# Kernel optimization log

Measured on AMD Instinct MI355X. Metric: run time of the kernel, lower is better.

Reference implementation:

```python
import jax, jax.numpy as jnp
import numpy as np

_DIMS = [15, 30, 60, 90, 120, 90, 60, 30, 15, 10, 5, 1]


def setup_inputs() -> dict:
    key = jax.random.key(0)
    keys = jax.random.split(key, 1 + 2 * 11)
    inp = {"x": jax.random.normal(keys[0], (524288, 15), dtype=jnp.float32)}
    for i in range(11):
        fan_in, fan_out = _DIMS[i], _DIMS[i + 1]
        bound = 1.0 / np.sqrt(fan_in)
        inp[f"W{i+1}"] = jax.random.uniform(keys[1 + 2 * i], (fan_out, fan_in), minval=-bound, maxval=bound, dtype=jnp.float32)
        inp[f"b{i+1}"] = jax.random.uniform(keys[2 + 2 * i], (fan_out,), minval=-bound, maxval=bound, dtype=jnp.float32)
    return inp


def reference(x, W1, b1, W2, b2, W3, b3, W4, b4, W5, b5, W6, b6, W7, b7, W8, b8, W9, b9, W10, b10, W11, b11):
    Ws = [W1, W2, W3, W4, W5, W6, W7, W8, W9, W10, W11]
    bs = [b1, b2, b3, b4, b5, b6, b7, b8, b9, b10, b11]
    h = x
    # 10 Linear+ReLU layers, funnel 15->30->60->90->120->90->60->30->15->10->5
    for W, b in zip(Ws[:-1], bs[:-1]):
        h = jax.nn.relu(h @ W.T + b)
    # final Linear 5->1 + sigmoid
    return jax.nn.sigmoid(h @ Ws[-1].T + bs[-1])
```

## Files before the change

### kernel.cpp

```cpp
#include <hip/hip_runtime.h>
#include <math.h>


using bf16x8 = __attribute__((ext_vector_type(8))) short;
using f32x4  = __attribute__((ext_vector_type(4))) float;
using u16x8  = __attribute__((ext_vector_type(8))) unsigned short;
using u32x2  = __attribute__((ext_vector_type(2))) unsigned;
typedef __bf16 bf16x2_t __attribute__((ext_vector_type(2)));

namespace {
constexpr int NL = 11;
constexpr int IN_[NL]   = {15, 30, 60, 90, 120, 90, 60, 30, 15, 10, 5};
constexpr int OUT_[NL]  = {30, 60, 90, 120, 90, 60, 30, 15, 10, 5, 1};
constexpr int KP_[NL]   = {32, 32, 64, 96, 128, 96, 64, 32, 32, 32, 32};
constexpr int NP_[NL]   = {32, 64, 96, 128, 96, 64, 32, 16, 16, 16, 16};
constexpr int WOFF_[NL] = {0, 1024, 3072, 9216, 21504, 33792, 39936, 41984, 42496, 43008, 43520};
constexpr int WTOT      = 44032;
constexpr int ACT_OFF   = WTOT;
constexpr int WAVES     = 16;
constexpr int THREADS   = WAVES * 64;
constexpr int ROWS_PER_WAVE  = 16;
constexpr int ROWS_PER_BLOCK = WAVES * ROWS_PER_WAVE;
constexpr int ARENA     = 2048;
constexpr int LDS_BYTES = (WTOT + WAVES * ARENA) * 2;
}

__device__ __forceinline__ unsigned short f2bf(float f) {
    unsigned u = __float_as_uint(f);
    u += 0x7fffu + ((u >> 16) & 1u);
    return (unsigned short)(u >> 16);
}

__device__ __forceinline__ unsigned pk2(float a, float b) {
#if __has_builtin(__builtin_amdgcn_cvt_pk_bf16_f32)
    return __builtin_bit_cast(unsigned, __builtin_amdgcn_cvt_pk_bf16_f32(a, b));
#else
    bf16x2_t c;
    c[0] = (__bf16)a;
    c[1] = (__bf16)b;
    return __builtin_bit_cast(unsigned, c);
#endif
}

template <int L>
__device__ __forceinline__ void stage_w(const float* __restrict__ W,
                                        const float* __restrict__ B,
                                        short* wlds, int tid) {
    constexpr int KP = KP_[L], NP = NP_[L], INl = IN_[L], OUTl = OUT_[L];
    constexpr int NKT = KP / 32;
    for (int idx = tid; idx < NP * KP; idx += THREADS) {
        const int f    = idx >> 9;
        const int t    = idx & 511;
        const int quad = t >> 7;
        const int colc = (t >> 3) & 15;
        const int j    = t & 7;
        const int mt   = f / NKT;
        const int kt   = f - mt * NKT;
        const int m    = mt * 16 + colc;
        const int k    = kt * 32 + quad * 8 + j;
        float v = 0.f;
        if (m < OUTl) {
            if (k < INl) v = W[m * INl + k];
            else if (k == INl) v = B[m];
            else if (k == INl + 1) {
                float hf = __builtin_bit_cast(float, (unsigned)f2bf(B[m]) << 16);
                v = B[m] - hf;
            }
        } else if (m == OUTl || m == OUTl + 1) {
            if (k == INl) v = 1.f;
        }
        wlds[WOFF_[L] + idx] = (short)f2bf(v);
    }
}

template <int L>
__device__ __forceinline__ void layer_fwd(const short* __restrict__ wlds,
                                          short* buf, int col, int quad) {
    constexpr int KP   = KP_[L];
    constexpr int NP   = NP_[L];
    constexpr int NKT  = KP / 32;
    constexpr int NMT  = NP / 16;
    const short* wl = wlds + WOFF_[L];
    const int fo = quad * 128 + col * 8;

    f32x4 acc[NMT];
#pragma unroll
    for (int mt = 0; mt < NMT; ++mt)
        acc[mt] = f32x4{0.f, 0.f, 0.f, 0.f};

#pragma unroll
    for (int kt = 0; kt < NKT; ++kt) {
        bf16x8 b0 = *(const bf16x8*)(buf + kt * 512 + fo);
#pragma unroll
        for (int mt = 0; mt < NMT; ++mt) {
            bf16x8 af = *(const bf16x8*)(wl + (mt * NKT + kt) * 512 + fo);
            acc[mt] = __builtin_amdgcn_mfma_f32_16x16x32_bf16(af, b0, acc[mt], 0, 0, 0);
        }
    }
#pragma unroll
    for (int mt = 0; mt < NMT; ++mt) {
        const int wbase = (mt >> 1) * 512 + ((mt & 1) * 2 + (quad >> 1)) * 128 + col * 8 + (quad & 1) * 4;
        u32x2 o;
        o[0] = pk2(fmaxf(acc[mt][0], 0.f), fmaxf(acc[mt][1], 0.f));
        o[1] = pk2(fmaxf(acc[mt][2], 0.f), fmaxf(acc[mt][3], 0.f));
        *(u32x2*)(buf + wbase) = o;
    }
}

template <int L, int NF>
__device__ __forceinline__ void layer_fwd_pre(const bf16x8 (&wf)[NF],
                                              short* buf, int col, int quad) {
    constexpr int KP  = KP_[L];
    constexpr int NP  = NP_[L];
    constexpr int NKT = KP / 32;
    constexpr int NMT = NP / 16;
    static_assert(NF == NKT * NMT, "frag count mismatch");
    const int fo = quad * 128 + col * 8;

    f32x4 acc[NMT];
#pragma unroll
    for (int mt = 0; mt < NMT; ++mt)
        acc[mt] = f32x4{0.f, 0.f, 0.f, 0.f};

#pragma unroll
    for (int kt = 0; kt < NKT; ++kt) {
        bf16x8 b0 = *(const bf16x8*)(buf + kt * 512 + fo);
#pragma unroll
        for (int mt = 0; mt < NMT; ++mt)
            acc[mt] = __builtin_amdgcn_mfma_f32_16x16x32_bf16(wf[mt * NKT + kt], b0, acc[mt], 0, 0, 0);
    }
#pragma unroll
    for (int mt = 0; mt < NMT; ++mt) {
        const int wbase = (mt >> 1) * 512 + ((mt & 1) * 2 + (quad >> 1)) * 128 + col * 8 + (quad & 1) * 4;
        u32x2 o;
        o[0] = pk2(fmaxf(acc[mt][0], 0.f), fmaxf(acc[mt][1], 0.f));
        o[1] = pk2(fmaxf(acc[mt][2], 0.f), fmaxf(acc[mt][3], 0.f));
        *(u32x2*)(buf + wbase) = o;
    }
}

__device__ __forceinline__ void layer_one(bf16x8 af, short* buf, int col, int quad) {
    const int fo = quad * 128 + col * 8;
    bf16x8 b0 = *(const bf16x8*)(buf + fo);
    f32x4 a0 = f32x4{0.f, 0.f, 0.f, 0.f};
    a0 = __builtin_amdgcn_mfma_f32_16x16x32_bf16(af, b0, a0, 0, 0, 0);
    const int wbase = (quad >> 1) * 128 + col * 8 + (quad & 1) * 4;
    u32x2 o0;
    o0[0] = pk2(fmaxf(a0[0], 0.f), fmaxf(a0[1], 0.f));
    o0[1] = pk2(fmaxf(a0[2], 0.f), fmaxf(a0[3], 0.f));
    *(u32x2*)(buf + wbase) = o0;
    if (quad == 0) buf[256 + col * 8] = (short)0x3F80;
}

__device__ __forceinline__ float4 ld4(const float* p) {
    float4 t;
    __builtin_memcpy(&t, p, 16);
    return t;
}

__device__ __forceinline__ void fetch_x(const float* __restrict__ x, int row0,
                                        int col, int quad, float4& a0) {
    const float* r0 = x + (long)(row0 + col) * 15;
    if (quad < 3) {
        a0 = ld4(r0 + quad * 4);
    } else {
        float4 t0 = ld4(r0 + 11);
        a0 = make_float4(t0.y, t0.z, t0.w, 1.f);
    }
}

__device__ __forceinline__ void stage_x(short* buf, float4 a0, int col, int quad) {
    const int off = (quad >> 1) * 128 + col * 8 + (quad & 1) * 4;
    u32x2 o0;
    o0[0] = pk2(a0.x, a0.y); o0[1] = pk2(a0.z, a0.w);
    *(u32x2*)(buf + off) = o0;
    if (quad == 0) buf[256 + col * 8] = (short)0x3F80;
}

extern "C" __global__ void __launch_bounds__(THREADS, 4)
mlp_fused(const float* __restrict__ x,
          const float* __restrict__ W0,  const float* __restrict__ B0,
          const float* __restrict__ W1,  const float* __restrict__ B1,
          const float* __restrict__ W2,  const float* __restrict__ B2,
          const float* __restrict__ W3,  const float* __restrict__ B3,
          const float* __restrict__ W4,  const float* __restrict__ B4,
          const float* __restrict__ W5,  const float* __restrict__ B5,
          const float* __restrict__ W6,  const float* __restrict__ B6,
          const float* __restrict__ W7,  const float* __restrict__ B7,
          const float* __restrict__ W8,  const float* __restrict__ B8,
          const float* __restrict__ W9,  const float* __restrict__ B9,
          const float* __restrict__ W10, const float* __restrict__ B10,
          float* __restrict__ out, int nchunks) {
    extern __shared__ short smem[];
    short* wlds = smem;
    short* act  = smem + ACT_OFF;

    const int tid = threadIdx.x;

    stage_w<0>(W0, B0, wlds, tid);
    stage_w<1>(W1, B1, wlds, tid);
    stage_w<2>(W2, B2, wlds, tid);
    stage_w<3>(W3, B3, wlds, tid);
    stage_w<4>(W4, B4, wlds, tid);
    stage_w<5>(W5, B5, wlds, tid);
    stage_w<6>(W6, B6, wlds, tid);
    stage_w<7>(W7, B7, wlds, tid);
    stage_w<8>(W8, B8, wlds, tid);
    stage_w<9>(W9, B9, wlds, tid);
    stage_w<10>(W10, B10, wlds, tid);
    __syncthreads();

    const int wave = tid >> 6;
    const int lane = tid & 63;
    const int col  = lane & 15;
    const int quad = lane >> 4;
    short* buf = act + wave * ARENA;
    const int fo = quad * 128 + col * 8;

    {
        u16x8 z = {0, 0, 0, 0, 0, 0, 0, 0};
#pragma unroll
        for (int i = 0; i < 4; ++i)
            *(u16x8*)(buf + (lane + i * 64) * 8) = z;
    }

    const bf16x8 w7  = *(const bf16x8*)(wlds + WOFF_[7]  + fo);
    const bf16x8 w8  = *(const bf16x8*)(wlds + WOFF_[8]  + fo);
    const bf16x8 w9  = *(const bf16x8*)(wlds + WOFF_[9]  + fo);
    const bf16x8 w10 = *(const bf16x8*)(wlds + WOFF_[10] + fo);

    bf16x8 wf2[12];
#pragma unroll
    for (int i = 0; i < 12; ++i)
        wf2[i] = *(const bf16x8*)(wlds + WOFF_[2] + i * 512 + fo);

    int chunk = blockIdx.x;
    float4 xa;
    if (chunk < nchunks)
        fetch_x(x, chunk * ROWS_PER_BLOCK + wave * ROWS_PER_WAVE, col, quad, xa);

    for (; chunk < nchunks; chunk += gridDim.x) {
        const int row0 = chunk * ROWS_PER_BLOCK + wave * ROWS_PER_WAVE;
        stage_x(buf, xa, col, quad);

        const int nxt = chunk + gridDim.x;
        if (nxt < nchunks)
            fetch_x(x, nxt * ROWS_PER_BLOCK + wave * ROWS_PER_WAVE, col, quad, xa);

        layer_fwd<0>(wlds, buf, col, quad);
        layer_fwd<1>(wlds, buf, col, quad);
        layer_fwd_pre<2, 12>(wf2, buf, col, quad);
        layer_fwd<3>(wlds, buf, col, quad);
        layer_fwd<4>(wlds, buf, col, quad);
        layer_fwd<5>(wlds, buf, col, quad);
        layer_fwd<6>(wlds, buf, col, quad);
        layer_one(w7, buf, col, quad);
        layer_one(w8, buf, col, quad);
        layer_one(w9, buf, col, quad);

        {
            bf16x8 b0 = *(const bf16x8*)(buf + fo);
            f32x4 a0 = f32x4{0.f, 0.f, 0.f, 0.f};
            a0 = __builtin_amdgcn_mfma_f32_16x16x32_bf16(w10, b0, a0, 0, 0, 0);
            if (quad == 0)
                out[row0 + col] = 1.f / (1.f + __expf(-a0[0]));
        }
    }
}

extern "C" void kernel_launch(void* const* d_in, const int* in_sizes, int n_in,
                              void* d_out, int out_size, void* d_ws, size_t ws_size,
                              hipStream_t stream) {
    (void)n_in; (void)d_ws; (void)ws_size; (void)out_size;
    const float* x = (const float*)d_in[0];
    const float* W[11];
    const float* B[11];
    for (int i = 0; i < 11; ++i) {
        W[i] = (const float*)d_in[1 + 2 * i];
        B[i] = (const float*)d_in[2 + 2 * i];
    }
    const int nrows   = in_sizes[0] / 15;
    const int nchunks = nrows / ROWS_PER_BLOCK;

    hipFuncSetAttribute((const void*)mlp_fused,
                        hipFuncAttributeMaxDynamicSharedMemorySize, LDS_BYTES);

    mlp_fused<<<dim3(256), dim3(THREADS), LDS_BYTES, stream>>>(
        x,
        W[0], B[0], W[1], B[1], W[2], B[2], W[3], B[3], W[4], B[4],
        W[5], B[5], W[6], B[6], W[7], B[7], W[8], B[8], W[9], B[9],
        W[10], B[10],
        (float*)d_out, nchunks);
}
```

Measured before the change: 177.6 us.

## Pair waves to share 32-row activation tiles and split output tiles

Each pair of waves now works on a shared 32-row activation arena instead of one wave owning 16 rows. Within a pair, each wave computes half of a layer's output tiles for both 16-row groups, so every weight fragment read from LDS feeds two MFMAs. The aim is to halve weight LDS traffic per row and halve the layer-2 register-resident weight fragments. The cost is two block-wide __syncthreads per wide layer across 16 waves, which serialises the waves and can stall MFMA issue.

```diff
diff --git a/kernel.cpp b/kernel.cpp
--- a/kernel.cpp
+++ b/kernel.cpp
@@ -19,10 +19,11 @@
 constexpr int ACT_OFF   = WTOT;
 constexpr int WAVES     = 16;
 constexpr int THREADS   = WAVES * 64;
-constexpr int ROWS_PER_WAVE  = 16;
-constexpr int ROWS_PER_BLOCK = WAVES * ROWS_PER_WAVE;
-constexpr int ARENA     = 2048;
-constexpr int LDS_BYTES = (WTOT + WAVES * ARENA) * 2;
+constexpr int PAIRS     = WAVES / 2;
+constexpr int ROWS_PER_PAIR  = 32;
+constexpr int ROWS_PER_BLOCK = PAIRS * ROWS_PER_PAIR;
+constexpr int ARENA     = 4096;
+constexpr int LDS_BYTES = (WTOT + PAIRS * ARENA) * 2;
 }
 
 __device__ __forceinline__ unsigned short f2bf(float f) {
@@ -74,82 +75,100 @@
 }
 
 template <int L>
-__device__ __forceinline__ void layer_fwd(const short* __restrict__ wlds,
-                                          short* buf, int col, int quad) {
+__device__ __forceinline__ void layer_pair(const short* __restrict__ wl,
+                                           short* buf, int col, int quad, int sub) {
     constexpr int KP   = KP_[L];
     constexpr int NP   = NP_[L];
     constexpr int NKT  = KP / 32;
     constexpr int NMT  = NP / 16;
-    const short* wl = wlds + WOFF_[L];
+    constexpr int NMH  = NMT / 2;
+    constexpr int NKTN = KP_[L + 1] / 32;
     const int fo = quad * 128 + col * 8;
 
-    f32x4 acc[NMT];
-#pragma unroll
-    for (int mt = 0; mt < NMT; ++mt)
-        acc[mt] = f32x4{0.f, 0.f, 0.f, 0.f};
+    f32x4 acc[NMH][2];
+#pragma unroll
+    for (int m = 0; m < NMH; ++m)
+#pragma unroll
+        for (int b = 0; b < 2; ++b)
+            acc[m][b] = f32x4{0.f, 0.f, 0.f, 0.f};
 
 #pragma unroll
     for (int kt = 0; kt < NKT; ++kt) {
         bf16x8 b0 = *(const bf16x8*)(buf + kt * 512 + fo);
-#pragma unroll
-        for (int mt = 0; mt < NMT; ++mt) {
+        bf16x8 b1 = *(const bf16x8*)(buf + (NKT + kt) * 512 + fo);
+#pragma unroll
+        for (int m = 0; m < NMH; ++m) {
+            const int mt = sub * NMH + m;
             bf16x8 af = *(const bf16x8*)(wl + (mt * NKT + kt) * 512 + fo);
-            acc[mt] = __builtin_amdgcn_mfma_f32_16x16x32_bf16(af, b0, acc[mt], 0, 0, 0);
-        }
-    }
-#pragma unroll
-    for (int mt = 0; mt < NMT; ++mt) {
+            acc[m][0] = __builtin_amdgcn_mfma_f32_16x16x32_bf16(af, b0, acc[m][0], 0, 0, 0);
+            acc[m][1] = __builtin_amdgcn_mfma_f32_16x16x32_bf16(af, b1, acc[m][1], 0, 0, 0);
+        }
+    }
+    __syncthreads();
+#pragma unroll
+    for (int m = 0; m < NMH; ++m) {
+        const int mt = sub * NMH + m;
         const int wbase = (mt >> 1) * 512 + ((mt & 1) * 2 + (quad >> 1)) * 128 + col * 8 + (quad & 1) * 4;
-        u32x2 o;
-        o[0] = pk2(fmaxf(acc[mt][0], 0.f), fmaxf(acc[mt][1], 0.f));
-        o[1] = pk2(fmaxf(acc[mt][2], 0.f), fmaxf(acc[mt][3], 0.f));
-        *(u32x2*)(buf + wbase) = o;
-    }
-}
-
-template <int L, int NF>
-__device__ __forceinline__ void layer_fwd_pre(const bf16x8 (&wf)[NF],
-                                              short* buf, int col, int quad) {
-    constexpr int KP  = KP_[L];
-    constexpr int NP  = NP_[L];
-    constexpr int NKT = KP / 32;
-    constexpr int NMT = NP / 16;
-    static_assert(NF == NKT * NMT, "frag count mismatch");
+#pragma unroll
+        for (int b = 0; b < 2; ++b) {
+            u32x2 o;
+            o[0] = pk2(fmaxf(acc[m][b][0], 0.f), fmaxf(acc[m][b][1], 0.f));
+            o[1] = pk2(fmaxf(acc[m][b][2], 0.f), fmaxf(acc[m][b][3], 0.f));
+            *(u32x2*)(buf + b * NKTN * 512 + wbase) = o;
+        }
+    }
+    __syncthreads();
+}
+
+__device__ __forceinline__ void layer2_pair(const bf16x8 (&wf)[6],
+                                            short* buf, int col, int quad, int sub) {
+    constexpr int NKT = 2, NMH = 3, NKTN = 3;
     const int fo = quad * 128 + col * 8;
-
-    f32x4 acc[NMT];
-#pragma unroll
-    for (int mt = 0; mt < NMT; ++mt)
-        acc[mt] = f32x4{0.f, 0.f, 0.f, 0.f};
-
+    f32x4 acc[NMH][2];
+#pragma unroll
+    for (int m = 0; m < NMH; ++m)
+#pragma unroll
+        for (int b = 0; b < 2; ++b)
+            acc[m][b] = f32x4{0.f, 0.f, 0.f, 0.f};
 #pragma unroll
     for (int kt = 0; kt < NKT; ++kt) {
         bf16x8 b0 = *(const bf16x8*)(buf + kt * 512 + fo);
-#pragma unroll
-        for (int mt = 0; mt < NMT; ++mt)
-            acc[mt] = __builtin_amdgcn_mfma_f32_16x16x32_bf16(wf[mt * NKT + kt], b0, acc[mt], 0, 0, 0);
-    }
-#pragma unroll
-    for (int mt = 0; mt < NMT; ++mt) {
+        bf16x8 b1 = *(const bf16x8*)(buf + (NKT + kt) * 512 + fo);
+#pragma unroll
+        for (int m = 0; m < NMH; ++m) {
+            acc[m][0] = __builtin_amdgcn_mfma_f32_16x16x32_bf16(wf[m * NKT + kt], b0, acc[m][0], 0, 0, 0);
+            acc[m][1] = __builtin_amdgcn_mfma_f32_16x16x32_bf16(wf[m * NKT + kt], b1, acc[m][1], 0, 0, 0);
+        }
+    }
+    __syncthreads();
+#pragma unroll
+    for (int m = 0; m < NMH; ++m) {
+        const int mt = sub * NMH + m;
         const int wbase = (mt >> 1) * 512 + ((mt & 1) * 2 + (quad >> 1)) * 128 + col * 8 + (quad & 1) * 4;
-        u32x2 o;
-        o[0] = pk2(fmaxf(acc[mt][0], 0.f), fmaxf(acc[mt][1], 0.f));
-        o[1] = pk2(fmaxf(acc[mt][2], 0.f), fmaxf(acc[mt][3], 0.f));
-        *(u32x2*)(buf + wbase) = o;
-    }
-}
-
-__device__ __forceinline__ void layer_one(bf16x8 af, short* buf, int col, int quad) {
+#pragma unroll
+        for (int b = 0; b < 2; ++b) {
+            u32x2 o;
+            o[0] = pk2(fmaxf(acc[m][b][0], 0.f), fmaxf(acc[m][b][1], 0.f));
+            o[1] = pk2(fmaxf(acc[m][b][2], 0.f), fmaxf(acc[m][b][3], 0.f));
+            *(u32x2*)(buf + b * NKTN * 512 + wbase) = o;
+        }
+    }
+    __syncthreads();
+}
+
+__device__ __forceinline__ void layer_one_half(bf16x8 af, short* buf,
+                                               int col, int quad, int sub) {
+    short* h = buf + sub * 512;
     const int fo = quad * 128 + col * 8;
-    bf16x8 b0 = *(const bf16x8*)(buf + fo);
+    bf16x8 b0 = *(const bf16x8*)(h + fo);
     f32x4 a0 = f32x4{0.f, 0.f, 0.f, 0.f};
     a0 = __builtin_amdgcn_mfma_f32_16x16x32_bf16(af, b0, a0, 0, 0, 0);
     const int wbase = (quad >> 1) * 128 + col * 8 + (quad & 1) * 4;
     u32x2 o0;
     o0[0] = pk2(fmaxf(a0[0], 0.f), fmaxf(a0[1], 0.f));
     o0[1] = pk2(fmaxf(a0[2], 0.f), fmaxf(a0[3], 0.f));
-    *(u32x2*)(buf + wbase) = o0;
-    if (quad == 0) buf[256 + col * 8] = (short)0x3F80;
+    *(u32x2*)(h + wbase) = o0;
+    if (quad == 0) h[256 + col * 8] = (short)0x3F80;
 }
 
 __device__ __forceinline__ float4 ld4(const float* p) {
@@ -169,12 +188,14 @@
     }
 }
 
-__device__ __forceinline__ void stage_x(short* buf, float4 a0, int col, int quad) {
+__device__ __forceinline__ void stage_x(short* buf, float4 a0,
+                                        int col, int quad, int sub) {
+    short* h = buf + sub * 512;
     const int off = (quad >> 1) * 128 + col * 8 + (quad & 1) * 4;
     u32x2 o0;
     o0[0] = pk2(a0.x, a0.y); o0[1] = pk2(a0.z, a0.w);
-    *(u32x2*)(buf + off) = o0;
-    if (quad == 0) buf[256 + col * 8] = (short)0x3F80;
+    *(u32x2*)(h + off) = o0;
+    if (quad == 0) h[256 + col * 8] = (short)0x3F80;
 }
 
 extern "C" __global__ void __launch_bounds__(THREADS, 4)
@@ -214,14 +235,16 @@
     const int lane = tid & 63;
     const int col  = lane & 15;
     const int quad = lane >> 4;
-    short* buf = act + wave * ARENA;
+    const int pair = wave >> 1;
+    const int sub  = wave & 1;
+    short* buf = act + pair * ARENA;
     const int fo = quad * 128 + col * 8;
 
     {
         u16x8 z = {0, 0, 0, 0, 0, 0, 0, 0};
 #pragma unroll
         for (int i = 0; i < 4; ++i)
-            *(u16x8*)(buf + (lane + i * 64) * 8) = z;
+            *(u16x8*)(buf + sub * 2048 + (lane + i * 64) * 8) = z;
     }
 
     const bf16x8 w7  = *(const bf16x8*)(wlds + WOFF_[7]  + fo);
@@ -229,37 +252,41 @@
     const bf16x8 w9  = *(const bf16x8*)(wlds + WOFF_[9]  + fo);
     const bf16x8 w10 = *(const bf16x8*)(wlds + WOFF_[10] + fo);
 
-    bf16x8 wf2[12];
-#pragma unroll
-    for (int i = 0; i < 12; ++i)
-        wf2[i] = *(const bf16x8*)(wlds + WOFF_[2] + i * 512 + fo);
+    bf16x8 wf2[6];
+#pragma unroll
+    for (int m = 0; m < 3; ++m)
+#pragma unroll
+        for (int kt = 0; kt < 2; ++kt)
+            wf2[m * 2 + kt] = *(const bf16x8*)(wlds + WOFF_[2] + ((sub * 3 + m) * 2 + kt) * 512 + fo);
 
     int chunk = blockIdx.x;
     float4 xa;
     if (chunk < nchunks)
-        fetch_x(x, chunk * ROWS_PER_BLOCK + wave * ROWS_PER_WAVE, col, quad, xa);
+        fetch_x(x, chunk * ROWS_PER_BLOCK + pair * ROWS_PER_PAIR + sub * 16, col, quad, xa);
 
     for (; chunk < nchunks; chunk += gridDim.x) {
-        const int row0 = chunk * ROWS_PER_BLOCK + wave * ROWS_PER_WAVE;
-        stage_x(buf, xa, col, quad);
+        const int row0 = chunk * ROWS_PER_BLOCK + pair * ROWS_PER_PAIR + sub * 16;
+        stage_x(buf, xa, col, quad, sub);
 
         const int nxt = chunk + gridDim.x;
         if (nxt < nchunks)
-            fetch_x(x, nxt * ROWS_PER_BLOCK + wave * ROWS_PER_WAVE, col, quad, xa);
-
-        layer_fwd<0>(wlds, buf, col, quad);
-        layer_fwd<1>(wlds, buf, col, quad);
-        layer_fwd_pre<2, 12>(wf2, buf, col, quad);
-        layer_fwd<3>(wlds, buf, col, quad);
-        layer_fwd<4>(wlds, buf, col, quad);
-        layer_fwd<5>(wlds, buf, col, quad);
-        layer_fwd<6>(wlds, buf, col, quad);
-        layer_one(w7, buf, col, quad);
-        layer_one(w8, buf, col, quad);
-        layer_one(w9, buf, col, quad);
+            fetch_x(x, nxt * ROWS_PER_BLOCK + pair * ROWS_PER_PAIR + sub * 16, col, quad, xa);
+
+        __syncthreads();
+
+        layer_pair<0>(wlds + WOFF_[0], buf, col, quad, sub);
+        layer_pair<1>(wlds + WOFF_[1], buf, col, quad, sub);
+        layer2_pair(wf2, buf, col, quad, sub);
+        layer_pair<3>(wlds + WOFF_[3], buf, col, quad, sub);
+        layer_pair<4>(wlds + WOFF_[4], buf, col, quad, sub);
+        layer_pair<5>(wlds + WOFF_[5], buf, col, quad, sub);
+        layer_pair<6>(wlds + WOFF_[6], buf, col, quad, sub);
+        layer_one_half(w7, buf, col, quad, sub);
+        layer_one_half(w8, buf, col, quad, sub);
+        layer_one_half(w9, buf, col, quad, sub);
 
         {
-            bf16x8 b0 = *(const bf16x8*)(buf + fo);
+            bf16x8 b0 = *(const bf16x8*)(buf + sub * 512 + fo);
             f32x4 a0 = f32x4{0.f, 0.f, 0.f, 0.f};
             a0 = __builtin_amdgcn_mfma_f32_16x16x32_bf16(w10, b0, a0, 0, 0, 0);
             if (quad == 0)
```

New measurement: 189.1 us. 1.06x slower.
